# Performance work log

Measured on AMD Instinct MI355X. Metric: run time of the kernel, lower is better.

The kernel has to match this reference:

```python
import jax, jax.numpy as jnp
import numpy as np

D_MODEL = 512
N_HEADS = 8
D_K = D_MODEL // N_HEADS


def setup_inputs() -> dict:
    key = jax.random.key(0)
    ks = jax.random.split(key, 12)
    B, S = 2, 4096
    std = 1.0 / np.sqrt(D_MODEL)
    inp = {
        "q": jax.random.normal(ks[0], (B, S, D_MODEL), jnp.float32),
        "k": jax.random.normal(ks[1], (B, S, D_MODEL), jnp.float32),
        "v": jax.random.normal(ks[2], (B, S, D_MODEL), jnp.float32),
        "Wq": jax.random.normal(ks[3], (D_MODEL, D_MODEL), jnp.float32) * std,
        "bq": jnp.zeros((D_MODEL,), jnp.float32),
        "Wk": jax.random.normal(ks[4], (D_MODEL, D_MODEL), jnp.float32) * std,
        "bk": jnp.zeros((D_MODEL,), jnp.float32),
        "Wv": jax.random.normal(ks[5], (D_MODEL, D_MODEL), jnp.float32) * std,
        "bv": jnp.zeros((D_MODEL,), jnp.float32),
        "Wo": jax.random.normal(ks[6], (D_MODEL, D_MODEL), jnp.float32) * std,
        "bo": jnp.zeros((D_MODEL,), jnp.float32),
        # torch init: ones
        "time_decay": jnp.ones((1, N_HEADS, 1, 1), jnp.float32) * 0.01,
        "scale": jnp.ones((1,), jnp.float32),
    }
    return inp


def reference(q, k, v, Wq, bq, Wk, bk, Wv, bv, Wo, bo, time_decay, scale):
    B, S, _ = q.shape
    # projections (torch Linear: x @ W.T + b), reshape to [B, H, S, d_k]
    def proj(x, W, b):
        y = x @ W.T + b
        return y.reshape(B, -1, N_HEADS, D_K).transpose(0, 2, 1, 3)

    qh = proj(q, Wq, bq)
    kh = proj(k, Wk, bk)
    vh = proj(v, Wv, bv)

    # scores: [B, H, Sq, Sk]
    scores = jnp.einsum("bhqd,bhkd->bhqk", qh, kh) / np.sqrt(D_K)
    scores = scores * scale
    # exponential decay over absolute key position (per-head learnable rate)
    pos = jnp.arange(S, dtype=scores.dtype)  # key positions
    decay = jnp.exp(-time_decay * jnp.abs(pos)[None, None, None, :])  # [1,H,1,Sk]
    scores = scores * decay

    attn = jax.nn.softmax(scores, axis=-1)
    context = jnp.einsum("bhqk,bhkd->bhqd", attn, vh)
    context = context.transpose(0, 2, 1, 3).reshape(B, S, D_MODEL)
    out = context @ Wo.T + bo
    return out
```

## Files before the change

kernel.cpp:

```cpp
#include <hip/hip_runtime.h>
#include <hip/hip_bf16.h>
#include <stdint.h>

typedef __attribute__((ext_vector_type(8))) __bf16 bf16x8;
typedef __attribute__((ext_vector_type(4))) float f32x4;
typedef __attribute__((ext_vector_type(16))) float f32x16;
typedef __attribute__((ext_vector_type(8))) unsigned short ushort8;
typedef __attribute__((ext_vector_type(4))) unsigned short ushort4v;
typedef __attribute__((ext_vector_type(2))) unsigned int uint2v;
typedef __attribute__((ext_vector_type(4))) unsigned int uint4v;

__device__ __forceinline__ unsigned short bfbits(float x) {
    __bf16 b = (__bf16)x;
    return __builtin_bit_cast(unsigned short, b);
}
__device__ __forceinline__ float bf2f_u(unsigned short u) {
    return __builtin_bit_cast(float, (unsigned int)u << 16);
}

__device__ __forceinline__ f32x4 mfma16(bf16x8 a, bf16x8 b, f32x4 c) {
    return __builtin_amdgcn_mfma_f32_16x16x32_bf16(a, b, c, 0, 0, 0);
}
__device__ __forceinline__ f32x16 mfma32(bf16x8 a, bf16x8 b, f32x16 c) {
    return __builtin_amdgcn_mfma_f32_32x32x16_bf16(a, b, c, 0, 0, 0);
}

__device__ __forceinline__ unsigned int cvtpk(float lo, float hi) {
    unsigned int r;
    asm("v_cvt_pk_bf16_f32 %0, %1, %2" : "=v"(r) : "v"(lo), "v"(hi));
    return r;
}

__device__ __forceinline__ float lanepull(float src, int srcl) {
    return __builtin_bit_cast(float,
        __builtin_amdgcn_ds_bpermute(srcl * 4, __builtin_bit_cast(int, src)));
}

__device__ __forceinline__ void gload16(const void* g, void* l) {
    __builtin_amdgcn_global_load_lds(
        (const __attribute__((address_space(1))) unsigned int*)g,
        (__attribute__((address_space(3))) unsigned int*)l, 16, 0, 0);
}

__device__ __forceinline__ f32x16 zero16() {
    f32x16 r;
    #pragma unroll
    for (int i = 0; i < 16; i++) r[i] = 0.f;
    return r;
}

__device__ __forceinline__ int tail_tiles(float tdh, float scale) {
    float cut = 5.3f + __logf(fmaxf(scale, 1e-20f));
    cut = fmaxf(cut, 0.f);
    tdh = fmaxf(tdh, 1e-8f);
    int kt = (int)ceilf(cut / (tdh * 64.f));
    if (kt < 1) kt = 1;
    if (kt > 64) kt = 64;
    return kt;
}

__global__ __launch_bounds__(256) void wconv(
    const float* __restrict__ Wq, const float* __restrict__ Wk,
    const float* __restrict__ Wv, const float* __restrict__ Wo,
    unsigned short* __restrict__ Wbf)
{
    const int t    = blockIdx.x * 256 + threadIdx.x;
    const int slab = t >> 15;
    const int off8 = t & 32767;
    const float* src = (slab == 0) ? Wq : (slab == 1) ? Wk : (slab == 2) ? Wv : Wo;
    float4 a = ((const float4*)(src + off8 * 8))[0];
    float4 b = ((const float4*)(src + off8 * 8))[1];
    uint4v pk = { cvtpk(a.x, a.y), cvtpk(a.z, a.w), cvtpk(b.x, b.y), cvtpk(b.z, b.w) };
    *(uint4v*)(Wbf + (size_t)slab * 262144 + off8 * 8) = pk;
}

__global__ __launch_bounds__(256) void gemm_qkv(
    const float* __restrict__ q, const float* __restrict__ k, const float* __restrict__ v,
    const unsigned short* __restrict__ Wbf,
    const float* __restrict__ bq, const float* __restrict__ bk, const float* __restrict__ bv,
    const float* __restrict__ td, const float* __restrict__ sc,
    unsigned short* __restrict__ Qh, unsigned short* __restrict__ Kh,
    unsigned short* __restrict__ Vt)
{
    __shared__ __align__(16) char ALDS[2][8192];

    const int id  = blockIdx.x;
    const int nid = (id & 7) * 192 + (id >> 3);
    const int z   = nid / 512;
    const int rem = nid & 511;
    const int bm  = rem >> 2;
    const int bn  = rem & 3;

    const float* A0   = (z == 0) ? q  : (z == 1) ? k  : v;
    const float* bias = (z == 0) ? bq : (z == 1) ? bk : bv;

    const int tid  = threadIdx.x;
    const int lane = tid & 63;
    const int w    = tid >> 6;
    const int wm   = w >> 1, wn = w & 1;
    const int l15  = lane & 15;
    const int g    = lane >> 4;

    const int lr = lane >> 3;
    const int lc = ((lane & 7) * 16) ^ (lr << 4);
    const char* asrc[2];
    #pragma unroll
    for (int j = 0; j < 2; j++)
        asrc[j] = (const char*)A0 + (size_t)(bm * 64 + w * 16 + j * 8 + lr) * 2048 + lc;
    int adst[2];
    #pragma unroll
    for (int j = 0; j < 2; j++) adst[j] = w * 2048 + j * 1024;

    const unsigned short* Bp[4];
    #pragma unroll
    for (int n = 0; n < 4; n++)
        Bp[n] = Wbf + (size_t)z * 262144
              + (size_t)(bn * 128 + wn * 64 + n * 16 + l15) * 512 + g * 8;

    f32x4 acc[2][4];
    #pragma unroll
    for (int m = 0; m < 2; m++)
        #pragma unroll
        for (int n = 0; n < 4; n++)
            acc[m][n] = (f32x4){0.f, 0.f, 0.f, 0.f};

    const int asw = (l15 & 7) << 4;
    const int c0  = (g * 32) ^ asw;

    #pragma unroll
    for (int j = 0; j < 2; j++) gload16(asrc[j], ALDS[0] + adst[j]);
    bf16x8 BA[4], BB[4];
    #pragma unroll
    for (int n = 0; n < 4; n++) BA[n] = *(const bf16x8*)Bp[n];

#define QKV_ITER(CUR, KK, BC, BN)                                                  \
    {                                                                              \
        asm volatile("s_waitcnt vmcnt(0)" ::: "memory");                           \
        __syncthreads();                                                           \
        if ((KK) < 15) {                                                           \
            _Pragma("unroll")                                                      \
            for (int j = 0; j < 2; j++)                                            \
                gload16(asrc[j] + (size_t)((KK) + 1) * 128,                        \
                        ALDS[(CUR) ^ 1] + adst[j]);                                \
            _Pragma("unroll")                                                      \
            for (int n = 0; n < 4; n++)                                            \
                BN[n] = *(const bf16x8*)(Bp[n] + (size_t)((KK) + 1) * 32);         \
        }                                                                          \
        bf16x8 af[2];                                                              \
        _Pragma("unroll")                                                          \
        for (int m = 0; m < 2; m++) {                                              \
            const char* base = ALDS[CUR] + (wm * 32 + m * 16 + l15) * 128;         \
            f32x4 v0 = *(const f32x4*)(base + c0);                                 \
            f32x4 v1 = *(const f32x4*)(base + (c0 ^ 16));                          \
            uint4v pk = { cvtpk(v0.x, v0.y), cvtpk(v0.z, v0.w),                    \
                          cvtpk(v1.x, v1.y), cvtpk(v1.z, v1.w) };                  \
            af[m] = __builtin_bit_cast(bf16x8, pk);                                \
        }                                                                          \
        __builtin_amdgcn_s_setprio(1);                                             \
        _Pragma("unroll")                                                          \
        for (int m = 0; m < 2; m++)                                                \
            _Pragma("unroll")                                                      \
            for (int n = 0; n < 4; n++)                                            \
                acc[m][n] = mfma16(af[m], BC[n], acc[m][n]);                       \
        __builtin_amdgcn_s_setprio(0);                                             \
    }

    #pragma unroll 1
    for (int t = 0; t < 8; ++t) {
        QKV_ITER(0, 2 * t, BA, BB)
        QKV_ITER(1, 2 * t + 1, BB, BA)
    }
#undef QKV_ITER

    const float coefL = sc[0] * 0.125f * 1.44269504f;

    #pragma unroll
    for (int m = 0; m < 2; m++) {
        const int grow0 = bm * 64 + wm * 32 + m * 16 + (g << 2);
        #pragma unroll
        for (int n = 0; n < 4; n++) {
            const int gcol = bn * 128 + wn * 64 + n * 16 + l15;
            const float bv2 = bias[gcol];
            f32x4 c = acc[m][n];
            const int b = grow0 >> 12, s0 = grow0 & 4095;
            const int h = gcol >> 6, dk = gcol & 63;
            if (z == 0) {
                const size_t base = ((size_t)(b * 8 + h) * 4096 + s0) * 64 + dk;
                #pragma unroll
                for (int r = 0; r < 4; r++)
                    Qh[base + (size_t)r * 64] = bfbits((c[r] + bv2) * coefL);
            } else if (z == 1) {
                const float tdh = td[h];
                const size_t base = ((size_t)(b * 8 + h) * 4096 + s0) * 64 + dk;
                #pragma unroll
                for (int r = 0; r < 4; r++)
                    Kh[base + (size_t)r * 64] = bfbits((c[r] + bv2) * __expf(-tdh * (float)(s0 + r)));
            } else {
                ushort4v pk = { bfbits(c[0] + bv2), bfbits(c[1] + bv2),
                                bfbits(c[2] + bv2), bfbits(c[3] + bv2) };
                *(ushort4v*)&Vt[((size_t)(b * 8 + h) * 64 + dk) * 4096 + s0] = pk;
            }
        }
    }
}

__global__ __launch_bounds__(256) void gemm_out(
    const unsigned short* __restrict__ Actx, const unsigned short* __restrict__ Wob,
    const float* __restrict__ bias, float* __restrict__ Out)
{
    __shared__ __align__(16) char ALDS[2][16384];

    const int id  = blockIdx.x;
    const int nid = (id & 7) * 64 + (id >> 3);
    const int bm  = nid >> 3;
    const int bn  = nid & 7;

    const int tid  = threadIdx.x;
    const int lane = tid & 63;
    const int w    = tid >> 6;
    const int wm   = w >> 1, wn = w & 1;
    const int l15  = lane & 15;
    const int g    = lane >> 4;

    const int lr  = lane >> 3;
    const int lc  = ((lane & 7) * 16) ^ (lr << 4);
    const char* asrc[4];
    #pragma unroll
    for (int j = 0; j < 4; j++)
        asrc[j] = (const char*)Actx + (size_t)(bm * 128 + w * 32 + j * 8 + lr) * 1024 + lc;
    int adst[4];
    #pragma unroll
    for (int j = 0; j < 4; j++) adst[j] = w * 4096 + j * 1024;

    const unsigned short* Bp[2];
    #pragma unroll
    for (int n = 0; n < 2; n++)
        Bp[n] = Wob + (size_t)(bn * 64 + wn * 32 + n * 16 + l15) * 512 + g * 8;

    f32x4 acc[4][2];
    #pragma unroll
    for (int m = 0; m < 4; m++)
        #pragma unroll
        for (int n = 0; n < 2; n++)
            acc[m][n] = (f32x4){0.f, 0.f, 0.f, 0.f};

    const int arow = l15;
    const int asw  = (arow & 7) << 4;

    #pragma unroll
    for (int j = 0; j < 4; j++) gload16(asrc[j], ALDS[0] + adst[j]);
    bf16x8 BA[2][2], BB[2][2];
    #pragma unroll
    for (int n = 0; n < 2; n++) {
        BA[n][0] = *(const bf16x8*)Bp[n];
        BA[n][1] = *(const bf16x8*)(Bp[n] + 32);
    }

#define OUT_ITER(CUR, KK, BC, BN)                                                  \
    {                                                                              \
        asm volatile("s_waitcnt vmcnt(0)" ::: "memory");                           \
        __syncthreads();                                                           \
        if ((KK) < 7) {                                                            \
            _Pragma("unroll")                                                      \
            for (int j = 0; j < 4; j++)                                            \
                gload16(asrc[j] + (size_t)((KK) + 1) * 128,                        \
                        ALDS[(CUR) ^ 1] + adst[j]);                                \
            _Pragma("unroll")                                                      \
            for (int n = 0; n < 2; n++) {                                          \
                BN[n][0] = *(const bf16x8*)(Bp[n] + (size_t)((KK) + 1) * 64);      \
                BN[n][1] = *(const bf16x8*)(Bp[n] + (size_t)((KK) + 1) * 64 + 32); \
            }                                                                      \
        }                                                                          \
        bf16x8 af[4][2];                                                           \
        _Pragma("unroll")                                                          \
        for (int m = 0; m < 4; m++) {                                              \
            const char* base = ALDS[CUR] + (wm * 64 + m * 16 + arow) * 128;        \
            af[m][0] = *(const bf16x8*)(base + ((g * 16) ^ asw));                  \
            af[m][1] = *(const bf16x8*)(base + ((64 + g * 16) ^ asw));             \
        }                                                                          \
        __builtin_amdgcn_s_setprio(1);                                             \
        _Pragma("unroll")                                                          \
        for (int m = 0; m < 4; m++)                                                \
            _Pragma("unroll")                                                      \
            for (int n = 0; n < 2; n++) {                                          \
                acc[m][n] = mfma16(af[m][0], BC[n][0], acc[m][n]);                 \
                acc[m][n] = mfma16(af[m][1], BC[n][1], acc[m][n]);                 \
            }                                                                      \
        __builtin_amdgcn_s_setprio(0);                                             \
    }

    #pragma unroll 1
    for (int t = 0; t < 4; ++t) {
        OUT_ITER(0, 2 * t, BA, BB)
        OUT_ITER(1, 2 * t + 1, BB, BA)
    }
#undef OUT_ITER

    #pragma unroll
    for (int m = 0; m < 4; m++) {
        const int grow0 = bm * 128 + wm * 64 + m * 16 + (g << 2);
        #pragma unroll
        for (int n = 0; n < 2; n++) {
            const int gcol = bn * 64 + wn * 32 + n * 16 + l15;
            const float bv2 = bias[gcol];
            f32x4 c = acc[m][n];
            #pragma unroll
            for (int r = 0; r < 4; r++)
                Out[(size_t)(grow0 + r) * 512 + gcol] = c[r] + bv2;
        }
    }
}

__global__ __launch_bounds__(512) void tail_pre(
    const unsigned short* __restrict__ Kh, const unsigned short* __restrict__ Vt,
    const float* __restrict__ td, const float* __restrict__ sc,
    unsigned short* __restrict__ Mt, float* __restrict__ SumV, float* __restrict__ KsL)
{
    __shared__ __align__(16) char KLDS[2][8192];
    __shared__ float redM[4][32][32];
    __shared__ float redv[64];
    __shared__ float redk[64];

    const int blk  = blockIdx.x;
    const int bh   = blk >> 1;
    const int half = blk & 1;
    const int h    = bh & 7;
    const int tid  = threadIdx.x;
    const int w    = tid >> 6;
    const int lane = tid & 63;
    const int l31  = lane & 31, hl = lane >> 5;
    const int d2q  = w & 1, d1q = (w >> 1) & 1, ksub = w >> 2;

    const int KT  = tail_tiles(td[h], sc[0]);
    const int K0  = KT * 64;
    const int nk  = 4096 - K0;
    const int kh0 = ((nk >> 1) + 63) & ~63;
    const int kcnt = half ? (nk - kh0) : kh0;
    const int kbeg = K0 + half * kh0;
    const int nch  = kcnt >> 6;

    const int lr = lane >> 3;
    const int r8 = (w * 8 + lr) & 7;
    const char* ksrc = (const char*)Kh + (size_t)(bh * 4096 + kbeg + w * 8 + lr) * 128
                     + (((lane & 7) * 16) ^ (r8 << 4));
    const int kdst = w * 1024;

    const unsigned short* Vp = Vt + (size_t)(bh * 64 + d2q * 32 + l31) * 4096 + kbeg;

    f32x16 macc = zero16();
    float sumv = 0.f, ksum = 0.f;

    if (nch > 0) gload16(ksrc, KLDS[0] + kdst);

    #pragma unroll 1
    for (int ch = 0; ch < nch; ++ch) {
        asm volatile("s_waitcnt vmcnt(0)" ::: "memory");
        __syncthreads();
        if (ch + 1 < nch)
            gload16(ksrc + (size_t)(ch + 1) * 8192, KLDS[(ch + 1) & 1] + kdst);
        const char* kb = KLDS[ch & 1];

        #pragma unroll
        for (int mf = 0; mf < 2; mf++) {
            const int kloc0 = ksub * 32 + mf * 16 + hl * 8;
            ushort8 kbv;
            #pragma unroll
            for (int e = 0; e < 8; e++) {
                const int row = kloc0 + e;
                kbv[e] = *(const unsigned short*)(kb + row * 128
                          + ((d1q * 64 + l31 * 2) ^ ((row & 7) << 4)));
            }
            if (d2q == 0) {
                #pragma unroll
                for (int e = 0; e < 8; e++) ksum += bf2f_u(kbv[e]);
            }
            bf16x8 av = *(const bf16x8*)(Vp + ch * 64 + kloc0);
            if (d1q == 0) {
                ushort8 au = __builtin_bit_cast(ushort8, av);
                #pragma unroll
                for (int e = 0; e < 8; e++) sumv += bf2f_u(au[e]);
            }
            macc = mfma32(av, __builtin_bit_cast(bf16x8, kbv), macc);
        }
    }

    sumv += __shfl_xor(sumv, 32);
    ksum += __shfl_xor(ksum, 32);

    const int quad = d2q * 2 + d1q;
    __syncthreads();
    if (ksub == 0) {
        #pragma unroll
        for (int r = 0; r < 16; r++) {
            const int row = (r & 3) + 8 * (r >> 2) + 4 * hl;
            redM[quad][row][l31] = macc[r];
        }
        if (d1q == 0 && hl == 0) redv[d2q * 32 + l31] = sumv;
        if (d2q == 0 && hl == 0) redk[d1q * 32 + l31] = ksum;
    }
    __syncthreads();
    if (ksub == 1) {
        unsigned short* Mb = Mt + (size_t)half * 16 * 4096 + (size_t)bh * 4096;
        #pragma unroll
        for (int r = 0; r < 16; r++) {
            const int row = (r & 3) + 8 * (r >> 2) + 4 * hl;
            const float mv = (macc[r] + redM[quad][row][l31]) * 0.6931472f;
            Mb[(size_t)(d2q * 32 + row) * 64 + d1q * 32 + l31] = bfbits(mv);
        }
        if (d1q == 0 && hl == 0)
            SumV[half * 1024 + bh * 64 + d2q * 32 + l31] = sumv + redv[d2q * 32 + l31];
        if (d2q == 0 && hl == 0)
            KsL[half * 1024 + bh * 64 + d1q * 32 + l31] = (ksum + redk[d1q * 32 + l31]) * 0.6931472f;
    }
}

__global__ __launch_bounds__(256, 4) void attn_decay(
    const unsigned short* __restrict__ Qh, const unsigned short* __restrict__ Kh,
    const unsigned short* __restrict__ Vt, const float* __restrict__ td,
    const float* __restrict__ sc,
    const unsigned short* __restrict__ Mt, const float* __restrict__ SumV,
    const float* __restrict__ KsL, unsigned short* __restrict__ ctx)
{
    __shared__ __align__(16) char LDSB[32768];

    const int tid  = threadIdx.x;
    const int lane = tid & 63;
    const int w    = tid >> 6;
    const int qg   = w >> 1;
    const int ws   = w & 1;
    const int l31  = lane & 31;
    const int hl   = lane >> 5;

    const int i  = blockIdx.x;
    const int bh = ((i & 7) << 1) | ((i >> 9) & 1);
    const int qt = (i >> 3) & 63;
    const int h  = bh & 7;
    const int b  = bh >> 3;

    const int KT = tail_tiles(td[h], sc[0]);
    const int nk = 4096 - KT * 64;

    bf16x8 qf[4];
    {
        const unsigned short* Qp =
            Qh + ((size_t)bh * 4096 + qt * 64 + qg * 32 + l31) * 64 + hl * 8;
        #pragma unroll
        for (int c = 0; c < 4; c++)
            qf[c] = *(const bf16x8*)(Qp + c * 16);
    }

    f32x16 o0 = zero16(), o1 = zero16();
    float lp = 0.f;

    const char* kgp0; const char* kgp1; const char* vgp0; const char* vgp1;
    int ldsoff0, ldsoff1;
    {
        const size_t kbaseB = (size_t)bh * 4096 * 64 * 2;
        const size_t vbaseB = (size_t)bh * 64 * 4096 * 2;
        const int p0 = w * 2048 + lane * 16;
        const int r0 = p0 >> 7, c0 = p0 & 127, sw0 = (r0 & 7) << 4;
        const int p1 = w * 2048 + 1024 + lane * 16;
        const int r1 = p1 >> 7, c1 = p1 & 127, sw1 = (r1 & 7) << 4;
        kgp0 = (const char*)Kh + kbaseB + (size_t)r0 * 128  + (c0 ^ sw0);
        kgp1 = (const char*)Kh + kbaseB + (size_t)r1 * 128  + (c1 ^ sw1);
        vgp0 = (const char*)Vt + vbaseB + (size_t)r0 * 8192 + (c0 ^ sw0);
        vgp1 = (const char*)Vt + vbaseB + (size_t)r1 * 8192 + (c1 ^ sw1);
        ldsoff0 = w * 2048;
        ldsoff1 = w * 2048 + 1024;
    }
    gload16(kgp0, LDSB + ldsoff0);
    gload16(kgp1, LDSB + ldsoff1);
    gload16(vgp0, LDSB + 16384 + ldsoff0);
    gload16(vgp1, LDSB + 16384 + ldsoff1);
    kgp0 += 8192; kgp1 += 8192; vgp0 += 128; vgp1 += 128;

    const int krow = ws * 32 + l31;
    const int ksw  = (krow & 7) << 4;

#define ATTN_TILE(CUR, KT_IDX)                                                    \
    {                                                                             \
        asm volatile("s_waitcnt vmcnt(0)" ::: "memory");                          \
        __syncthreads();                                                          \
        if ((KT_IDX) + 1 < KT) {                                                  \
            gload16(kgp0, LDSB + ((CUR) ^ 1) * 8192 + ldsoff0);                   \
            gload16(kgp1, LDSB + ((CUR) ^ 1) * 8192 + ldsoff1);                   \
            gload16(vgp0, LDSB + 16384 + ((CUR) ^ 1) * 8192 + ldsoff0);           \
            gload16(vgp1, LDSB + 16384 + ((CUR) ^ 1) * 8192 + ldsoff1);           \
            kgp0 += 8192; kgp1 += 8192; vgp0 += 128; vgp1 += 128;                 \
        }                                                                         \
        const char* kb = LDSB + (CUR) * 8192;                                     \
        const char* vb = LDSB + 16384 + (CUR) * 8192;                             \
        f32x16 s = zero16();                                                      \
        __builtin_amdgcn_s_setprio(1);                                            \
        _Pragma("unroll")                                                         \
        for (int c = 0; c < 4; c++) {                                             \
            bf16x8 kf = *(const bf16x8*)(kb + krow * 128 + ((c * 32 + hl * 16) ^ ksw)); \
            s = mfma32(kf, qf[c], s);                                             \
        }                                                                         \
        __builtin_amdgcn_s_setprio(0);                                            \
        float p[16];                                                              \
        _Pragma("unroll")                                                         \
        for (int r = 0; r < 16; r++) {                                            \
            p[r] = __builtin_amdgcn_exp2f(s[r]);                                  \
            lp += p[r];                                                           \
        }                                                                         \
        unsigned int W0 = cvtpk(p[0], p[1]),   W1 = cvtpk(p[2], p[3]);            \
        unsigned int W2 = cvtpk(p[4], p[5]),   W3 = cvtpk(p[6], p[7]);            \
        unsigned int W4 = cvtpk(p[8], p[9]),   W5 = cvtpk(p[10], p[11]);          \
        unsigned int W6 = cvtpk(p[12], p[13]), W7 = cvtpk(p[14], p[15]);          \
        uint2v r02 = __builtin_amdgcn_permlane32_swap(W0, W2, false, false);      \
        uint2v r13 = __builtin_amdgcn_permlane32_swap(W1, W3, false, false);      \
        uint2v r46 = __builtin_amdgcn_permlane32_swap(W4, W6, false, false);      \
        uint2v r57 = __builtin_amdgcn_permlane32_swap(W5, W7, false, false);      \
        bf16x8 pa0 = __builtin_bit_cast(bf16x8, (uint4v){r02.x, r13.x, r02.y, r13.y}); \
        bf16x8 pa1 = __builtin_bit_cast(bf16x8, (uint4v){r46.x, r57.x, r46.y, r57.y}); \
        __builtin_amdgcn_s_setprio(1);                                            \
        {                                                                         \
            const int vr0  = l31;                                                 \
            const int vsw0 = (vr0 & 7) << 4;                                      \
            bf16x8 va = *(const bf16x8*)(vb + vr0 * 128 + ((ws * 64 + hl * 16) ^ vsw0));      \
            bf16x8 vb2 = *(const bf16x8*)(vb + vr0 * 128 + ((ws * 64 + 32 + hl * 16) ^ vsw0));\
            o0 = mfma32(pa0, va, o0);                                             \
            o0 = mfma32(pa1, vb2, o0);                                            \
            const int vr1  = 32 + l31;                                            \
            const int vsw1 = (vr1 & 7) << 4;                                      \
            bf16x8 vc = *(const bf16x8*)(vb + vr1 * 128 + ((ws * 64 + hl * 16) ^ vsw1));      \
            bf16x8 vd = *(const bf16x8*)(vb + vr1 * 128 + ((ws * 64 + 32 + hl * 16) ^ vsw1)); \
            o1 = mfma32(pa0, vc, o1);                                             \
            o1 = mfma32(pa1, vd, o1);                                             \
        }                                                                         \
        __builtin_amdgcn_s_setprio(0);                                            \
    }

    const int KT2 = KT >> 1;
    #pragma unroll 1
    for (int t = 0; t < KT2; ++t) {
        ATTN_TILE(0, 2 * t)
        ATTN_TILE(1, 2 * t + 1)
    }
    if (KT & 1) {
        ATTN_TILE(0, KT - 1)
    }
#undef ATTN_TILE

    if (ws == 0 && nk > 0) {
        float qk = 0.f;
        #pragma unroll
        for (int c = 0; c < 4; c++) {
            ushort8 qb = __builtin_bit_cast(ushort8, qf[c]);
            #pragma unroll
            for (int e = 0; e < 8; e++) {
                const int idx = c * 16 + hl * 8 + e;
                qk += bf2f_u(qb[e]) * (KsL[bh * 64 + idx] + KsL[1024 + bh * 64 + idx]);
            }
        }
        qk += __shfl_xor(qk, 32);
        if (hl == 0) lp += (float)nk + qk;

        #pragma unroll
        for (int half = 0; half < 2; half++) {
            const unsigned short* Mb = Mt + (size_t)half * 16 * 4096 + (size_t)bh * 4096;
            #pragma unroll
            for (int c = 0; c < 4; c++) {
                bf16x8 m0 = *(const bf16x8*)(Mb + (size_t)l31 * 64 + c * 16 + hl * 8);
                bf16x8 m1 = *(const bf16x8*)(Mb + (size_t)(32 + l31) * 64 + c * 16 + hl * 8);
                o0 = mfma32(qf[c], m0, o0);
                o1 = mfma32(qf[c], m1, o1);
            }
        }
        const float sv0 = SumV[bh * 64 + l31]      + SumV[1024 + bh * 64 + l31];
        const float sv1 = SumV[bh * 64 + 32 + l31] + SumV[1024 + bh * 64 + 32 + l31];
        #pragma unroll
        for (int r = 0; r < 16; r++) { o0[r] += sv0; o1[r] += sv1; }
    }

    float lw = lp + __shfl_xor(lp, 32);
    __syncthreads();
    float* lscr = (float*)(LDSB + 16384);
    if (lane < 32)
        lscr[(qg * 2 + ws) * 32 + lane] = lw;
    __syncthreads();
    const float pl2 = lscr[(qg * 2 + (ws ^ 1)) * 32 + l31];
    const float myscale = 1.f / (lw + pl2);
    #pragma unroll
    for (int rc = 0; rc < 4; rc++)
        #pragma unroll
        for (int j = 0; j < 4; j++) {
            const float a = lanepull(myscale, rc * 8 + hl * 4 + j);
            o0[rc * 4 + j] *= a;
            o1[rc * 4 + j] *= a;
        }
    __syncthreads();
    float* Oscr = (float*)(LDSB + qg * 8192);
    if (ws == 1) {
        #pragma unroll
        for (int reg = 0; reg < 16; reg++) {
            const int row = (reg & 3) + 8 * (reg >> 2) + 4 * hl;
            Oscr[row * 64 + l31]      = o0[reg];
            Oscr[row * 64 + 32 + l31] = o1[reg];
        }
    }
    __syncthreads();
    if (ws == 0) {
        #pragma unroll
        for (int reg = 0; reg < 16; reg++) {
            const int row = (reg & 3) + 8 * (reg >> 2) + 4 * hl;
            const float v0 = o0[reg] + Oscr[row * 64 + l31];
            const float v1 = o1[reg] + Oscr[row * 64 + 32 + l31];
            const int srow_ = qt * 64 + qg * 32 + row;
            const size_t idx = ((size_t)b * 4096 + srow_) * 512 + h * 64;
            ctx[idx + l31]      = bfbits(v0);
            ctx[idx + 32 + l31] = bfbits(v1);
        }
    }
}

extern "C" void kernel_launch(void* const* d_in, const int* in_sizes, int n_in,
                              void* d_out, int out_size, void* d_ws, size_t ws_size,
                              hipStream_t stream)
{
    (void)in_sizes; (void)n_in; (void)out_size; (void)ws_size;
    const float* q  = (const float*)d_in[0];
    const float* k  = (const float*)d_in[1];
    const float* v  = (const float*)d_in[2];
    const float* Wq = (const float*)d_in[3];
    const float* bq = (const float*)d_in[4];
    const float* Wk = (const float*)d_in[5];
    const float* bk = (const float*)d_in[6];
    const float* Wv = (const float*)d_in[7];
    const float* bv = (const float*)d_in[8];
    const float* Wo = (const float*)d_in[9];
    const float* bo = (const float*)d_in[10];
    const float* td = (const float*)d_in[11];
    const float* sc = (const float*)d_in[12];

    unsigned short* Qh  = (unsigned short*)d_ws;
    unsigned short* Kh  = Qh + (size_t)16 * 4096 * 64;
    unsigned short* Vt  = Kh + (size_t)16 * 4096 * 64;
    unsigned short* ctx = Vt + (size_t)16 * 4096 * 64;
    unsigned short* Wbf = ctx + (size_t)16 * 4096 * 64;

    unsigned short* Mt   = (unsigned short*)d_out;
    float*          SumV = (float*)((char*)d_out + 2 * 16 * 4096 * 2);
    float*          KsL  = SumV + 2 * 1024;

    wconv<<<dim3(512), 256, 0, stream>>>(Wq, Wk, Wv, Wo, Wbf);
    gemm_qkv<<<dim3(1536), 256, 0, stream>>>(q, k, v, Wbf, bq, bk, bv, td, sc, Qh, Kh, Vt);
    tail_pre<<<dim3(32), 512, 0, stream>>>(Kh, Vt, td, sc, Mt, SumV, KsL);
    attn_decay<<<dim3(1024), 256, 0, stream>>>(Qh, Kh, Vt, td, sc, Mt, SumV, KsL, ctx);
    gemm_out<<<dim3(512), 256, 0, stream>>>(ctx, Wbf + (size_t)3 * 262144, bo, (float*)d_out);
}
```

Baseline: 130.8 us.

## Triple-buffer QKV and output projection GEMMs with prefetch distance two

Both projection GEMM kernels move from double-buffered LDS to three LDS stages, prefetching A tiles and B registers two k-steps ahead. The full vmcnt(0) wait is replaced by a partial vmcnt wait so one stage's loads can still be in flight while the current stage computes, and the k-loops are fully unrolled. This aims to hide global load latency better. It costs more LDS per block, which may reduce occupancy, and more registers for the third B fragment set.

Measured after the change: 130.1 us. No clear change (-0.5%).

```diff
diff --git a/kernel.cpp b/kernel.cpp
--- a/kernel.cpp
+++ b/kernel.cpp
@@ -82,11 +82,11 @@
     unsigned short* __restrict__ Qh, unsigned short* __restrict__ Kh,
     unsigned short* __restrict__ Vt)
 {
-    __shared__ __align__(16) char ALDS[2][8192];
+    __shared__ __align__(16) char ALDS[3][8192];
 
     const int id  = blockIdx.x;
     const int nid = (id & 7) * 192 + (id >> 3);
-    const int z   = nid / 512;
+    const int z   = nid >> 9;
     const int rem = nid & 511;
     const int bm  = rem >> 2;
     const int bn  = rem & 3;
@@ -107,9 +107,7 @@
     #pragma unroll
     for (int j = 0; j < 2; j++)
         asrc[j] = (const char*)A0 + (size_t)(bm * 64 + w * 16 + j * 8 + lr) * 2048 + lc;
-    int adst[2];
-    #pragma unroll
-    for (int j = 0; j < 2; j++) adst[j] = w * 2048 + j * 1024;
+    const int adst0 = w * 2048, adst1 = w * 2048 + 1024;
 
     const unsigned short* Bp[4];
     #pragma unroll
@@ -127,29 +125,36 @@
     const int asw = (l15 & 7) << 4;
     const int c0  = (g * 32) ^ asw;
 
-    #pragma unroll
-    for (int j = 0; j < 2; j++) gload16(asrc[j], ALDS[0] + adst[j]);
-    bf16x8 BA[4], BB[4];
-    #pragma unroll
-    for (int n = 0; n < 4; n++) BA[n] = *(const bf16x8*)Bp[n];
-
-#define QKV_ITER(CUR, KK, BC, BN)                                                  \
+    bf16x8 B0[4], B1[4], B2[4];
+
+    gload16(asrc[0], ALDS[0] + adst0);
+    gload16(asrc[1], ALDS[0] + adst1);
+    #pragma unroll
+    for (int n = 0; n < 4; n++) B0[n] = *(const bf16x8*)Bp[n];
+    gload16(asrc[0] + 128, ALDS[1] + adst0);
+    gload16(asrc[1] + 128, ALDS[1] + adst1);
+    #pragma unroll
+    for (int n = 0; n < 4; n++) B1[n] = *(const bf16x8*)(Bp[n] + 32);
+
+#define QKV_ITER(KK, BC, BN)                                                       \
     {                                                                              \
-        asm volatile("s_waitcnt vmcnt(0)" ::: "memory");                           \
-        __syncthreads();                                                           \
-        if ((KK) < 15) {                                                           \
-            _Pragma("unroll")                                                      \
-            for (int j = 0; j < 2; j++)                                            \
-                gload16(asrc[j] + (size_t)((KK) + 1) * 128,                        \
-                        ALDS[(CUR) ^ 1] + adst[j]);                                \
+        if ((KK) == 15) { asm volatile("s_waitcnt vmcnt(0)" ::: "memory"); }       \
+        else            { asm volatile("s_waitcnt vmcnt(6)" ::: "memory"); }       \
+        __builtin_amdgcn_s_barrier();                                              \
+        __builtin_amdgcn_sched_barrier(0);                                         \
+        if ((KK) + 2 < 16) {                                                       \
+            gload16(asrc[0] + (size_t)((KK) + 2) * 128,                            \
+                    ALDS[((KK) + 2) % 3] + adst0);                                 \
+            gload16(asrc[1] + (size_t)((KK) + 2) * 128,                            \
+                    ALDS[((KK) + 2) % 3] + adst1);                                 \
             _Pragma("unroll")                                                      \
             for (int n = 0; n < 4; n++)                                            \
-                BN[n] = *(const bf16x8*)(Bp[n] + (size_t)((KK) + 1) * 32);         \
+                BN[n] = *(const bf16x8*)(Bp[n] + (size_t)((KK) + 2) * 32);         \
         }                                                                          \
         bf16x8 af[2];                                                              \
         _Pragma("unroll")                                                          \
         for (int m = 0; m < 2; m++) {                                              \
-            const char* base = ALDS[CUR] + (wm * 32 + m * 16 + l15) * 128;         \
+            const char* base = ALDS[(KK) % 3] + (wm * 32 + m * 16 + l15) * 128;    \
             f32x4 v0 = *(const f32x4*)(base + c0);                                 \
             f32x4 v1 = *(const f32x4*)(base + (c0 ^ 16));                          \
             uint4v pk = { cvtpk(v0.x, v0.y), cvtpk(v0.z, v0.w),                    \
@@ -165,11 +170,12 @@
         __builtin_amdgcn_s_setprio(0);                                             \
     }
 
-    #pragma unroll 1
-    for (int t = 0; t < 8; ++t) {
-        QKV_ITER(0, 2 * t, BA, BB)
-        QKV_ITER(1, 2 * t + 1, BB, BA)
-    }
+    QKV_ITER(0,  B0, B2)  QKV_ITER(1,  B1, B0)  QKV_ITER(2,  B2, B1)
+    QKV_ITER(3,  B0, B2)  QKV_ITER(4,  B1, B0)  QKV_ITER(5,  B2, B1)
+    QKV_ITER(6,  B0, B2)  QKV_ITER(7,  B1, B0)  QKV_ITER(8,  B2, B1)
+    QKV_ITER(9,  B0, B2)  QKV_ITER(10, B1, B0)  QKV_ITER(11, B2, B1)
+    QKV_ITER(12, B0, B2)  QKV_ITER(13, B1, B0)  QKV_ITER(14, B2, B1)
+    QKV_ITER(15, B0, B2)
 #undef QKV_ITER
 
     const float coefL = sc[0] * 0.125f * 1.44269504f;
@@ -208,7 +214,7 @@
     const unsigned short* __restrict__ Actx, const unsigned short* __restrict__ Wob,
     const float* __restrict__ bias, float* __restrict__ Out)
 {
-    __shared__ __align__(16) char ALDS[2][16384];
+    __shared__ __align__(16) char ALDS[3][16384];
 
     const int id  = blockIdx.x;
     const int nid = (id & 7) * 64 + (id >> 3);
@@ -222,8 +228,8 @@
     const int l15  = lane & 15;
     const int g    = lane >> 4;
 
-    const int lr  = lane >> 3;
-    const int lc  = ((lane & 7) * 16) ^ (lr << 4);
+    const int lr = lane >> 3;
+    const int lc = ((lane & 7) * 16) ^ (lr << 4);
     const char* asrc[4];
     #pragma unroll
     for (int j = 0; j < 4; j++)
@@ -244,37 +250,46 @@
         for (int n = 0; n < 2; n++)
             acc[m][n] = (f32x4){0.f, 0.f, 0.f, 0.f};
 
-    const int arow = l15;
-    const int asw  = (arow & 7) << 4;
+    const int asw = (l15 & 7) << 4;
+
+    bf16x8 B0[2][2], B1[2][2], B2[2][2];
 
     #pragma unroll
     for (int j = 0; j < 4; j++) gload16(asrc[j], ALDS[0] + adst[j]);
-    bf16x8 BA[2][2], BB[2][2];
     #pragma unroll
     for (int n = 0; n < 2; n++) {
-        BA[n][0] = *(const bf16x8*)Bp[n];
-        BA[n][1] = *(const bf16x8*)(Bp[n] + 32);
-    }
-
-#define OUT_ITER(CUR, KK, BC, BN)                                                  \
+        B0[n][0] = *(const bf16x8*)Bp[n];
+        B0[n][1] = *(const bf16x8*)(Bp[n] + 32);
+    }
+    #pragma unroll
+    for (int j = 0; j < 4; j++) gload16(asrc[j] + 128, ALDS[1] + adst[j]);
+    #pragma unroll
+    for (int n = 0; n < 2; n++) {
+        B1[n][0] = *(const bf16x8*)(Bp[n] + 64);
+        B1[n][1] = *(const bf16x8*)(Bp[n] + 96);
+    }
+
+#define OUT_ITER(KK, BC, BN)                                                       \
     {                                                                              \
-        asm volatile("s_waitcnt vmcnt(0)" ::: "memory");                           \
-        __syncthreads();                                                           \
-        if ((KK) < 7) {                                                            \
+        if ((KK) == 7) { asm volatile("s_waitcnt vmcnt(0)" ::: "memory"); }        \
+        else           { asm volatile("s_waitcnt vmcnt(8)" ::: "memory"); }        \
+        __builtin_amdgcn_s_barrier();                                              \
+        __builtin_amdgcn_sched_barrier(0);                                         \
+        if ((KK) + 2 < 8) {                                                        \
             _Pragma("unroll")                                                      \
             for (int j = 0; j < 4; j++)                                            \
-                gload16(asrc[j] + (size_t)((KK) + 1) * 128,                        \
-                        ALDS[(CUR) ^ 1] + adst[j]);                                \
+                gload16(asrc[j] + (size_t)((KK) + 2) * 128,                        \
+                        ALDS[((KK) + 2) % 3] + adst[j]);                           \
             _Pragma("unroll")                                                      \
             for (int n = 0; n < 2; n++) {                                          \
-                BN[n][0] = *(const bf16x8*)(Bp[n] + (size_t)((KK) + 1) * 64);      \
-                BN[n][1] = *(const bf16x8*)(Bp[n] + (size_t)((KK) + 1) * 64 + 32); \
+                BN[n][0] = *(const bf16x8*)(Bp[n] + (size_t)((KK) + 2) * 64);      \
+                BN[n][1] = *(const bf16x8*)(Bp[n] + (size_t)((KK) + 2) * 64 + 32); \
             }                                                                      \
         }                                                                          \
         bf16x8 af[4][2];                                                           \
         _Pragma("unroll")                                                          \
         for (int m = 0; m < 4; m++) {                                              \
-            const char* base = ALDS[CUR] + (wm * 64 + m * 16 + arow) * 128;        \
+            const char* base = ALDS[(KK) % 3] + (wm * 64 + m * 16 + l15) * 128;    \
             af[m][0] = *(const bf16x8*)(base + ((g * 16) ^ asw));                  \
             af[m][1] = *(const bf16x8*)(base + ((64 + g * 16) ^ asw));             \
         }                                                                          \
@@ -289,11 +304,9 @@
         __builtin_amdgcn_s_setprio(0);                                             \
     }
 
-    #pragma unroll 1
-    for (int t = 0; t < 4; ++t) {
-        OUT_ITER(0, 2 * t, BA, BB)
-        OUT_ITER(1, 2 * t + 1, BB, BA)
-    }
+    OUT_ITER(0, B0, B2)  OUT_ITER(1, B1, B0)  OUT_ITER(2, B2, B1)
+    OUT_ITER(3, B0, B2)  OUT_ITER(4, B1, B0)  OUT_ITER(5, B2, B1)
+    OUT_ITER(6, B0, B2)  OUT_ITER(7, B1, B0)
 #undef OUT_ITER
 
     #pragma unroll
```
